# Performance work log

Measured on AMD Instinct MI355X. Metric: run time of the kernel, lower is better.

## Reference

```python
import jax, jax.numpy as jnp
import numpy as np

N = 50000      # n_verts
E = 800000     # n_edges (avg degree 16)
C = 128        # in_channels
F_OUT = 128    # out_feats
H = 32         # metric_n_hidden
D = 3          # embedding_dim (tangent vectors in R^3)
N_FACES = 100000
EPS = 1e-8


def setup_inputs() -> dict:
    key = jax.random.key(0)
    ks = jax.random.split(key, 8)
    features = jax.random.normal(ks[0], (N, C), jnp.float32)
    vertices = jax.random.normal(ks[1], (N, 3), jnp.float32)
    edges = jax.random.randint(ks[2], (2, E), 0, N, dtype=jnp.int64)
    faces = jax.random.randint(ks[3], (N_FACES, 3), 0, N, dtype=jnp.int64)
    glorot = lambda k, sh: jax.random.normal(k, sh, jnp.float32) * np.float32(1.0 / np.sqrt(sh[0]))
    W1 = glorot(ks[4], (C, H))          # metric MLP layer 1
    b1 = jnp.zeros((H,), jnp.float32)
    W2 = glorot(ks[5], (H, D * D))      # metric MLP layer 2 -> per-vertex 3x3 metric
    b2 = jnp.zeros((D * D,), jnp.float32)
    weights = glorot(ks[6], (C, F_OUT))  # conv filter W
    bias = jax.random.uniform(ks[7], (F_OUT,), jnp.float32, -0.1, 0.1)
    return {"features": features, "vertices": vertices, "edges": edges, "faces": faces,
            "W1": W1, "b1": b1, "W2": W2, "b2": b2, "weights": weights, "bias": bias}


def reference(features, vertices, edges, faces, W1, b1, W2, b2, weights, bias):
    # Y = A X W + b, where A is a dynamic weighted adjacency built from a
    # per-vertex learned metric applied to edge tangent vectors (info='tangent').
    src, dst = edges[0], edges[1]
    # per-vertex metric: MLP(features) -> M_i in R^{3x3}, G_i = M_i^T M_i (PSD)
    h = jax.nn.relu(features @ W1 + b1)                      # [N, H]
    M = (h @ W2 + b2).reshape(-1, D, D)                      # [N, 3, 3]
    G = jnp.einsum('nki,nkj->nij', M, M)                     # [N, 3, 3] metric_per_vertex
    Ge = 0.5 * (G[src] + G[dst])                             # symmetric=True: w_ij == w_ji
    t = vertices[dst] - vertices[src]                        # [E, 3] tangent vectors
    q = jnp.einsum('ei,eij,ej->e', t, Ge, t)                 # squared metric length
    w = jnp.exp(-q)                                          # [E] edge weights
    # aggregation: out_i = sum_j A_ij (XW)_j with row-normalized A
    xw = features @ weights                                  # [N, F_OUT]
    msg = w[:, None] * xw[dst]                               # [E, F_OUT]
    agg = jax.ops.segment_sum(msg, src, num_segments=N)      # [N, F_OUT]
    rowsum = jax.ops.segment_sum(w, src, num_segments=N)     # [N]
    return agg / (rowsum[:, None] + EPS) + bias
```

## Files before the change

### kernel.cpp

```cpp
#include <hip/hip_runtime.h>
#include <hip/hip_bf16.h>

#define CIN  128
#define FOUT 128
#define HID  32
#define BIG_SH 7
#define BIGW  128
#define CAPBIN 2560
#define SUBW  32
#define NSUB  4
#define CAPSUB 704
#define EPSV 1e-8f

typedef __attribute__((ext_vector_type(8))) short bf16x8;
typedef __attribute__((ext_vector_type(4))) float f32x4;

__device__ inline short f2bf(float x) {
    union { float f; unsigned u; } v; v.f = x;
    unsigned r = v.u + 0x7fffu + ((v.u >> 16) & 1u);
    return (short)(r >> 16);
}
__device__ inline float bfbits2f(unsigned b) {
    union { unsigned u; float f; } v; v.u = b << 16;
    return v.f;
}

__global__ void prep_kernel(const float* __restrict__ Wc,
                            const float* __restrict__ W1,
                            const float* __restrict__ verts,
                            short* __restrict__ WcT,
                            short* __restrict__ W1T,
                            float* __restrict__ vertsP,
                            int* __restrict__ binctr,
                            int N, int nbins) {
    const int idx = blockIdx.x * 256 + threadIdx.x;
    if (idx < CIN * FOUT) {
        const int c = idx >> 7, k = idx & 127;
        WcT[c * CIN + k] = f2bf(Wc[k * FOUT + c]);
    }
    if (idx < HID * CIN) {
        const int c = idx >> 7, k = idx & 127;
        W1T[c * CIN + k] = f2bf(W1[k * HID + c]);
    }
    if (idx < N) {
        vertsP[idx * 4 + 0] = verts[idx * 3 + 0];
        vertsP[idx * 4 + 1] = verts[idx * 3 + 1];
        vertsP[idx * 4 + 2] = verts[idx * 3 + 2];
        vertsP[idx * 4 + 3] = 0.f;
    }
    if (idx < nbins) binctr[idx] = 0;
}

__global__ __launch_bounds__(256) void bin_kernel(const int* __restrict__ edges,
                                                  int* __restrict__ binctr,
                                                  unsigned* __restrict__ binbuf,
                                                  int E, int nbins) {
    __shared__ int cnt[512];
    __shared__ int base[512];
    const int tid = threadIdx.x;
    for (int b = tid; b < nbins; b += 256) cnt[b] = 0;
    __syncthreads();

    int ebin[16]; unsigned epack[16];
    const int e0 = blockIdx.x * 4096;
#pragma unroll
    for (int i = 0; i < 16; ++i) {
        const int e = e0 + i * 256 + tid;
        ebin[i] = -1;
        if (e < E) {
            const int s = edges[e];
            const int d = edges[E + e];
            ebin[i] = s >> BIG_SH;
            epack[i] = ((unsigned)(s & (BIGW - 1)) << 16) | (unsigned)d;
            atomicAdd(&cnt[ebin[i]], 1);
        }
    }
    __syncthreads();
    for (int b = tid; b < nbins; b += 256) {
        const int c = cnt[b];
        base[b] = c ? atomicAdd(&binctr[b], c) : 0;
        cnt[b] = 0;
    }
    __syncthreads();
#pragma unroll
    for (int i = 0; i < 16; ++i) {
        if (ebin[i] >= 0) {
            const int rk = base[ebin[i]] + atomicAdd(&cnt[ebin[i]], 1);
            if (rk < CAPBIN) binbuf[(size_t)ebin[i] * CAPBIN + rk] = epack[i];
        }
    }
}

__global__ __launch_bounds__(256) void vertex_mfma(
    const float* __restrict__ feat,
    const short* __restrict__ WcT,
    const short* __restrict__ W1T,
    const float* __restrict__ b1,
    const float* __restrict__ W2,
    const float* __restrict__ b2,
    float* __restrict__ Gp,
    unsigned short* __restrict__ xwb,
    int N) {
    __shared__ unsigned short xw_s[4][16][FOUT];
    __shared__ float h_lds[4][16][HID];
    __shared__ float M_lds[4][16][9];
    const int wid  = threadIdx.x >> 6;
    const int lane = threadIdx.x & 63;
    const int v0   = (blockIdx.x * 4 + wid) * 16;
    const int r    = lane & 15;
    const int hi   = lane >> 4;
    const int vr   = min(v0 + r, N - 1);

    bf16x8 a[4];
#pragma unroll
    for (int kt = 0; kt < 4; ++kt) {
        const float* src = feat + (size_t)vr * CIN + kt * 32 + hi * 8;
        const float4 f0 = ((const float4*)src)[0];
        const float4 f1 = ((const float4*)src)[1];
        bf16x8 t;
        t[0] = f2bf(f0.x); t[1] = f2bf(f0.y); t[2] = f2bf(f0.z); t[3] = f2bf(f0.w);
        t[4] = f2bf(f1.x); t[5] = f2bf(f1.y); t[6] = f2bf(f1.z); t[7] = f2bf(f1.w);
        a[kt] = t;
    }

#pragma unroll
    for (int ct = 0; ct < 8; ++ct) {
        f32x4 acc = {0.f, 0.f, 0.f, 0.f};
#pragma unroll
        for (int kt = 0; kt < 4; ++kt) {
            const bf16x8 b = *((const bf16x8*)(WcT + (size_t)(ct * 16 + r) * CIN + kt * 32 + hi * 8));
            acc = __builtin_amdgcn_mfma_f32_16x16x32_bf16(a[kt], b, acc, 0, 0, 0);
        }
#pragma unroll
        for (int reg = 0; reg < 4; ++reg)
            xw_s[wid][hi * 4 + reg][ct * 16 + r] = (unsigned short)f2bf(acc[reg]);
    }

#pragma unroll
    for (int row = 0; row < 16; ++row) {
        if (v0 + row < N) {
            const unsigned d = ((const unsigned*)xw_s[wid][row])[lane];
            ((unsigned*)(xwb + (size_t)(v0 + row) * FOUT))[lane] = d;
        }
    }

#pragma unroll
    for (int ct = 0; ct < 2; ++ct) {
        f32x4 acc = {0.f, 0.f, 0.f, 0.f};
#pragma unroll
        for (int kt = 0; kt < 4; ++kt) {
            const bf16x8 b = *((const bf16x8*)(W1T + (size_t)(ct * 16 + r) * CIN + kt * 32 + hi * 8));
            acc = __builtin_amdgcn_mfma_f32_16x16x32_bf16(a[kt], b, acc, 0, 0, 0);
        }
        const float bb = b1[ct * 16 + r];
#pragma unroll
        for (int reg = 0; reg < 4; ++reg)
            h_lds[wid][hi * 4 + reg][ct * 16 + r] = fmaxf(acc[reg] + bb, 0.f);
    }
    __syncthreads();

    for (int idx = lane; idx < 144; idx += 64) {
        const int v = idx / 9, t = idx - v * 9;
        float m = b2[t];
#pragma unroll
        for (int k = 0; k < HID; ++k)
            m = fmaf(h_lds[wid][v][k], W2[k * 9 + t], m);
        M_lds[wid][v][t] = m;
    }
    __syncthreads();

    for (int idx = lane; idx < 96; idx += 64) {
        const int v = idx / 6, t = idx - v * 6;
        const int i = (t >= 3) + (t >= 5);
        const int j = t - (t >= 3) * 2 - (t >= 5);
        float g = 0.f;
#pragma unroll
        for (int k = 0; k < 3; ++k)
            g += M_lds[wid][v][k * 3 + i] * M_lds[wid][v][k * 3 + j];
        if (v0 + v < N) Gp[(size_t)(v0 + v) * 8 + t] = g;
    }
}

__global__ __launch_bounds__(256) void agg_kernel(const int* __restrict__ binctr,
                                                  const unsigned* __restrict__ binbuf,
                                                  const float* __restrict__ vertsP,
                                                  const float* __restrict__ Gp,
                                                  const unsigned short* __restrict__ xwb,
                                                  const float* __restrict__ bias,
                                                  float* __restrict__ out,
                                                  int N) {
    __shared__ unsigned short dstS[CAPSUB];
    __shared__ float wS[CAPSUB];
    __shared__ int cnt[SUBW], off[SUBW], cnt2[SUBW];
    __shared__ float sG[SUBW * 8];
    __shared__ float sV[SUBW * 4];

    const int b   = blockIdx.x >> 2;
    const int sub = blockIdx.x & 3;
    const int v0  = (b << BIG_SH) + sub * SUBW;
    const int tid = threadIdx.x;

    if (tid < SUBW) { cnt[tid] = 0; cnt2[tid] = 0; }
    {
        const int v = v0 + (tid >> 3);
        sG[tid] = (v < N) ? Gp[(size_t)v * 8 + (tid & 7)] : 0.f;
        if (tid < SUBW * 4) {
            const int v2 = v0 + (tid >> 2);
            sV[tid] = (v2 < N) ? vertsP[(size_t)v2 * 4 + (tid & 3)] : 0.f;
        }
    }
    __syncthreads();

    const int n = min(binctr[b], CAPBIN);

    for (int i = tid; i < n; i += 256) {
        const unsigned p = binbuf[(size_t)b * CAPBIN + i];
        const int ls = (int)(p >> 16);
        if ((ls >> 5) == sub) atomicAdd(&cnt[ls & 31], 1);
    }
    __syncthreads();
    if (tid < SUBW) {
        int o = 0;
        for (int j = 0; j < tid; ++j) o += cnt[j];
        off[tid] = o;
    }
    __syncthreads();

    for (int i = tid; i < n; i += 256) {
        const unsigned p = binbuf[(size_t)b * CAPBIN + i];
        const int ls = (int)(p >> 16);
        if ((ls >> 5) != sub) continue;
        const int l = ls & 31;
        const int d = (int)(p & 0xffffu);

        const float4 vd = ((const float4*)vertsP)[d];
        const float4 ha = ((const float4*)(Gp + (size_t)d * 8))[0];
        const float2 hb = ((const float2*)(Gp + (size_t)d * 8 + 4))[0];
        const float* gs = &sG[l * 8];
        const float* vv = &sV[l * 4];
        const float t0 = vd.x - vv[0], t1 = vd.y - vv[1], t2 = vd.z - vv[2];
        const float g00 = gs[0] + ha.x, g01 = gs[1] + ha.y, g02 = gs[2] + ha.z;
        const float g11 = gs[3] + ha.w, g12 = gs[4] + hb.x, g22 = gs[5] + hb.y;
        const float q = 0.5f * (g00 * t0 * t0 + g11 * t1 * t1 + g22 * t2 * t2
                      + 2.f * (g01 * t0 * t1 + g02 * t0 * t2 + g12 * t1 * t2));
        const float w = __expf(-q);

        const int slot = off[l] + atomicAdd(&cnt2[l], 1);
        if (slot < CAPSUB) { dstS[slot] = (unsigned short)d; wS[slot] = w; }
    }
    __syncthreads();

    const int wid  = tid >> 6;
    const int lane = tid & 63;
    const float2 bb = ((const float2*)bias)[lane];

    for (int l = wid * 8; l < wid * 8 + 8; ++l) {
        const int v = v0 + l;
        if (v >= N) break;
        const int start = off[l];
        int deg = cnt[l];
        int m = CAPSUB - start; if (m < 0) m = 0; if (deg > m) deg = m;

        float ax = 0.f, ay = 0.f, wsum = 0.f;
        int k = 0;
        for (; k + 8 <= deg; k += 8) {
            int   d_[8]; float w_[8]; unsigned u_[8];
#pragma unroll
            for (int j = 0; j < 8; ++j) { d_[j] = dstS[start + k + j]; w_[j] = wS[start + k + j]; }
#pragma unroll
            for (int j = 0; j < 8; ++j) u_[j] = ((const unsigned*)(xwb + (size_t)d_[j] * FOUT))[lane];
#pragma unroll
            for (int j = 0; j < 8; ++j) {
                ax = fmaf(w_[j], bfbits2f(u_[j] & 0xffffu), ax);
                ay = fmaf(w_[j], bfbits2f(u_[j] >> 16), ay);
                wsum += w_[j];
            }
        }
        for (; k < deg; ++k) {
            const int   d0 = dstS[start + k];
            const float w0 = wS[start + k];
            const unsigned u0 = ((const unsigned*)(xwb + (size_t)d0 * FOUT))[lane];
            ax = fmaf(w0, bfbits2f(u0 & 0xffffu), ax);
            ay = fmaf(w0, bfbits2f(u0 >> 16), ay);
            wsum += w0;
        }

        const float inv = 1.f / (wsum + EPSV);
        float2 o;
        o.x = ax * inv + bb.x;
        o.y = ay * inv + bb.y;
        ((float2*)(out + (size_t)v * FOUT))[lane] = o;
    }
}

extern "C" void kernel_launch(void* const* d_in, const int* in_sizes, int n_in,
                              void* d_out, int out_size, void* d_ws, size_t ws_size,
                              hipStream_t stream) {
    const float* feat  = (const float*)d_in[0];
    const float* verts = (const float*)d_in[1];
    const int*   edges = (const int*)d_in[2];
    const float* W1    = (const float*)d_in[4];
    const float* b1    = (const float*)d_in[5];
    const float* W2    = (const float*)d_in[6];
    const float* b2    = (const float*)d_in[7];
    const float* Wc    = (const float*)d_in[8];
    const float* bias  = (const float*)d_in[9];

    const int N = in_sizes[0] / CIN;
    const int E = in_sizes[2] / 2;
    const int nbins = (N + BIGW - 1) >> BIG_SH;

    char* p = (char*)d_ws;
    auto alloc = [&](size_t bytes) {
        char* r = p;
        p += (bytes + 255) & ~(size_t)255;
        return r;
    };
    short*          WcT    = (short*)alloc((size_t)CIN * FOUT * sizeof(short));
    short*          W1T    = (short*)alloc((size_t)HID * CIN * sizeof(short));
    unsigned short* xwb    = (unsigned short*)alloc((size_t)N * FOUT * sizeof(short));
    float*          Gp     = (float*)alloc((size_t)N * 8 * sizeof(float));
    float*          vertsP = (float*)alloc((size_t)N * 4 * sizeof(float));
    unsigned*       binbuf = (unsigned*)alloc((size_t)nbins * CAPBIN * sizeof(unsigned));
    int*            binctr = (int*)alloc((size_t)nbins * sizeof(int));
    float*          out    = (float*)d_out;

    const int prep_n = (N > CIN * FOUT) ? N : CIN * FOUT;
    prep_kernel<<<(prep_n + 255) / 256, 256, 0, stream>>>(Wc, W1, verts, WcT, W1T, vertsP,
                                                          binctr, N, nbins);

    bin_kernel<<<(E + 4095) / 4096, 256, 0, stream>>>(edges, binctr, binbuf, E, nbins);

    const int nwaves = (N + 15) / 16;
    vertex_mfma<<<(nwaves + 3) / 4, 256, 0, stream>>>(feat, WcT, W1T, b1, W2, b2, Gp, xwb, N);

    agg_kernel<<<nbins * NSUB, 256, 0, stream>>>(binctr, binbuf, vertsP, Gp, xwb, bias, out, N);
}
```

Before: 103.0 us.

## Split bins into eight sub-blocks and use fixed per-vertex LDS slots

The aggregation kernel now handles 16 vertices per block instead of 32, so eight blocks share each bin. The separate counting pass, prefix scan and extra barriers are replaced by one pass that writes each edge into a fixed 40-entry slot array per vertex. This removes a full re-read of the bin and two synchronisations, and launches more blocks. In exchange, every block still scans the whole bin, so redundant bin reads double. Any vertex with more than 40 edges in a bin would be silently truncated.

After: 105.4 us. 1.02x slower.

```diff
diff --git a/kernel.cpp b/kernel.cpp
--- a/kernel.cpp
+++ b/kernel.cpp
@@ -7,9 +7,9 @@
 #define BIG_SH 7
 #define BIGW  128
 #define CAPBIN 2560
-#define SUBW  32
-#define NSUB  4
-#define CAPSUB 704
+#define SUBW  16
+#define NSUB  8
+#define CAPV  40
 #define EPSV 1e-8f
 
 typedef __attribute__((ext_vector_type(8))) short bf16x8;
@@ -189,25 +189,25 @@
                                                   const float* __restrict__ bias,
                                                   float* __restrict__ out,
                                                   int N) {
-    __shared__ unsigned short dstS[CAPSUB];
-    __shared__ float wS[CAPSUB];
-    __shared__ int cnt[SUBW], off[SUBW], cnt2[SUBW];
+    __shared__ unsigned short dloc[SUBW][CAPV];
+    __shared__ float wloc[SUBW][CAPV];
+    __shared__ int cnt[SUBW];
     __shared__ float sG[SUBW * 8];
     __shared__ float sV[SUBW * 4];
 
-    const int b   = blockIdx.x >> 2;
-    const int sub = blockIdx.x & 3;
+    const int b   = blockIdx.x >> 3;
+    const int sub = blockIdx.x & 7;
     const int v0  = (b << BIG_SH) + sub * SUBW;
     const int tid = threadIdx.x;
 
-    if (tid < SUBW) { cnt[tid] = 0; cnt2[tid] = 0; }
-    {
+    if (tid < SUBW) cnt[tid] = 0;
+    if (tid < SUBW * 8) {
         const int v = v0 + (tid >> 3);
         sG[tid] = (v < N) ? Gp[(size_t)v * 8 + (tid & 7)] : 0.f;
-        if (tid < SUBW * 4) {
-            const int v2 = v0 + (tid >> 2);
-            sV[tid] = (v2 < N) ? vertsP[(size_t)v2 * 4 + (tid & 3)] : 0.f;
-        }
+    }
+    if (tid < SUBW * 4) {
+        const int v2 = v0 + (tid >> 2);
+        sV[tid] = (v2 < N) ? vertsP[(size_t)v2 * 4 + (tid & 3)] : 0.f;
     }
     __syncthreads();
 
@@ -216,21 +216,8 @@
     for (int i = tid; i < n; i += 256) {
         const unsigned p = binbuf[(size_t)b * CAPBIN + i];
         const int ls = (int)(p >> 16);
-        if ((ls >> 5) == sub) atomicAdd(&cnt[ls & 31], 1);
-    }
-    __syncthreads();
-    if (tid < SUBW) {
-        int o = 0;
-        for (int j = 0; j < tid; ++j) o += cnt[j];
-        off[tid] = o;
-    }
-    __syncthreads();
-
-    for (int i = tid; i < n; i += 256) {
-        const unsigned p = binbuf[(size_t)b * CAPBIN + i];
-        const int ls = (int)(p >> 16);
-        if ((ls >> 5) != sub) continue;
-        const int l = ls & 31;
+        if ((ls >> 4) != sub) continue;
+        const int l = ls & 15;
         const int d = (int)(p & 0xffffu);
 
         const float4 vd = ((const float4*)vertsP)[d];
@@ -245,8 +232,8 @@
                       + 2.f * (g01 * t0 * t1 + g02 * t0 * t2 + g12 * t1 * t2));
         const float w = __expf(-q);
 
-        const int slot = off[l] + atomicAdd(&cnt2[l], 1);
-        if (slot < CAPSUB) { dstS[slot] = (unsigned short)d; wS[slot] = w; }
+        const int rk = atomicAdd(&cnt[l], 1);
+        if (rk < CAPV) { dloc[l][rk] = (unsigned short)d; wloc[l][rk] = w; }
     }
     __syncthreads();
 
@@ -254,19 +241,17 @@
     const int lane = tid & 63;
     const float2 bb = ((const float2*)bias)[lane];
 
-    for (int l = wid * 8; l < wid * 8 + 8; ++l) {
+    for (int l = wid * 4; l < wid * 4 + 4; ++l) {
         const int v = v0 + l;
         if (v >= N) break;
-        const int start = off[l];
-        int deg = cnt[l];
-        int m = CAPSUB - start; if (m < 0) m = 0; if (deg > m) deg = m;
+        const int deg = min(cnt[l], CAPV);
 
         float ax = 0.f, ay = 0.f, wsum = 0.f;
         int k = 0;
         for (; k + 8 <= deg; k += 8) {
             int   d_[8]; float w_[8]; unsigned u_[8];
 #pragma unroll
-            for (int j = 0; j < 8; ++j) { d_[j] = dstS[start + k + j]; w_[j] = wS[start + k + j]; }
+            for (int j = 0; j < 8; ++j) { d_[j] = dloc[l][k + j]; w_[j] = wloc[l][k + j]; }
 #pragma unroll
             for (int j = 0; j < 8; ++j) u_[j] = ((const unsigned*)(xwb + (size_t)d_[j] * FOUT))[lane];
 #pragma unroll
@@ -277,8 +262,8 @@
             }
         }
         for (; k < deg; ++k) {
-            const int   d0 = dstS[start + k];
-            const float w0 = wS[start + k];
+            const int   d0 = dloc[l][k];
+            const float w0 = wloc[l][k];
             const unsigned u0 = ((const unsigned*)(xwb + (size_t)d0 * FOUT))[lane];
             ax = fmaf(w0, bfbits2f(u0 & 0xffffu), ax);
             ay = fmaf(w0, bfbits2f(u0 >> 16), ay);
```
